# Performance work log

Hardware: AMD Instinct MI355X
Metric: run time of the kernel (lower is better)

The kernel has to match this reference:

```python
import jax, jax.numpy as jnp
import numpy as np

N = 100000      # nodes
E_RAND = 1500000
IN_DIM = 128
OUT_DIM = 128
H = 8
D = OUT_DIM // H  # 16 per-head dim
EPS = 1e-5


def _bn(x, gamma, beta):
    # BatchNorm1d, training mode: biased batch statistics over the node dim
    mu = jnp.mean(x, axis=0)
    var = jnp.mean((x - mu) ** 2, axis=0)
    return (x - mu) * jax.lax.rsqrt(var + EPS) * gamma + beta


def setup_inputs() -> dict:
    key = jax.random.key(0)
    ks = jax.random.split(key, 12)
    h = jax.random.normal(ks[0], (N, IN_DIM), dtype=jnp.float32)
    # edge list: random edges + self-loops so every dst has in-degree >= 1
    src_r = jax.random.randint(ks[1], (E_RAND,), 0, N, dtype=jnp.int32)
    dst_r = jax.random.randint(ks[2], (E_RAND,), 0, N, dtype=jnp.int32)
    loops = jnp.arange(N, dtype=jnp.int32)
    src = jnp.concatenate([loops, src_r])
    dst = jnp.concatenate([loops, dst_r])
    s = 1.0 / np.sqrt(IN_DIM)
    Wq = jax.random.normal(ks[3], (IN_DIM, OUT_DIM), dtype=jnp.float32) * s
    Wk = jax.random.normal(ks[4], (IN_DIM, OUT_DIM), dtype=jnp.float32) * s
    Wv = jax.random.normal(ks[5], (IN_DIM, OUT_DIM), dtype=jnp.float32) * s
    Wo = jax.random.normal(ks[6], (OUT_DIM, OUT_DIM), dtype=jnp.float32) * s
    bo = jnp.zeros((OUT_DIM,), dtype=jnp.float32)
    gamma1 = jnp.ones((OUT_DIM,), dtype=jnp.float32)
    beta1 = jnp.zeros((OUT_DIM,), dtype=jnp.float32)
    Wf1 = jax.random.normal(ks[7], (OUT_DIM, 2 * OUT_DIM), dtype=jnp.float32) * s
    bf1 = jnp.zeros((2 * OUT_DIM,), dtype=jnp.float32)
    Wf2 = jax.random.normal(ks[8], (2 * OUT_DIM, OUT_DIM), dtype=jnp.float32) * (1.0 / np.sqrt(2 * OUT_DIM))
    bf2 = jnp.zeros((OUT_DIM,), dtype=jnp.float32)
    gamma2 = jnp.ones((OUT_DIM,), dtype=jnp.float32)
    beta2 = jnp.zeros((OUT_DIM,), dtype=jnp.float32)
    return {"h": h, "Wq": Wq, "Wk": Wk, "Wv": Wv, "Wo": Wo, "bo": bo,
            "gamma1": gamma1, "beta1": beta1, "Wf1": Wf1, "bf1": bf1,
            "Wf2": Wf2, "bf2": bf2, "gamma2": gamma2, "beta2": beta2,
            "src": src, "dst": dst}


def reference(h, Wq, Wk, Wv, Wo, bo, gamma1, beta1, Wf1, bf1, Wf2, bf2,
              gamma2, beta2, src, dst):
    n = h.shape[0]
    Q = (h @ Wq).reshape(n, H, D)
    K = (h @ Wk).reshape(n, H, D)
    V = (h @ Wv).reshape(n, H, D)
    # per-edge score: (K[src] * Q[dst]).sum(-1), scaled exp with clamp
    score = jnp.sum(K[src] * Q[dst], axis=-1) / np.sqrt(D)   # [E, H]
    score = jnp.exp(jnp.clip(score, -5.0, 5.0))
    # weighted aggregation to dst nodes
    wV = jax.ops.segment_sum(V[src] * score[:, :, None], dst, num_segments=n)  # [N,H,D]
    z = jax.ops.segment_sum(score, dst, num_segments=n)                         # [N,H]
    attn = (wV / z[:, :, None]).reshape(n, OUT_DIM)
    # output projection + residual + batchnorm
    x = h + (attn @ Wo + bo)
    x = _bn(x, gamma1, beta1)
    # FFN + residual + batchnorm
    y = jax.nn.relu(x @ Wf1 + bf1) @ Wf2 + bf2
    x = _bn(x + y, gamma2, beta2)
    return x
```

## Files before the change

kernel.cpp:

```cpp
#include <hip/hip_runtime.h>

#define EPS 1e-5f
#define VSCALE 20.0f

typedef __attribute__((ext_vector_type(8))) short sh8;
typedef __attribute__((ext_vector_type(4))) float f4;
typedef __attribute__((ext_vector_type(2))) _Float16 h2f;

static __device__ __forceinline__ unsigned short f2b(float f) {
    union { float f; unsigned u; } v; v.f = f;
    unsigned r = v.u + 0x7FFF + ((v.u >> 16) & 1);
    return (unsigned short)(r >> 16);
}
static __device__ __forceinline__ float b2f(unsigned short b) {
    union { unsigned u; float f; } v; v.u = ((unsigned)b) << 16; return v.f;
}
static __device__ __forceinline__ unsigned pk2(float a, float b) {
    return (unsigned)f2b(a) | ((unsigned)f2b(b) << 16);
}
static __device__ __forceinline__ h2f u2h(unsigned u) {
    union { unsigned u; h2f h; } c; c.u = u; return c.h;
}
static __device__ __forceinline__ float dot2h(h2f a, h2f b, float c) {
#if __has_builtin(__builtin_amdgcn_fdot2)
    return __builtin_amdgcn_fdot2(a, b, c, false);
#else
    return (float)a.x * (float)b.x + (float)a.y * (float)b.y + c;
#endif
}
#if __has_builtin(__builtin_amdgcn_cvt_f32_ubyte0)
#define UB0(x) __builtin_amdgcn_cvt_f32_ubyte0(x)
#define UB1(x) __builtin_amdgcn_cvt_f32_ubyte1(x)
#define UB2(x) __builtin_amdgcn_cvt_f32_ubyte2(x)
#define UB3(x) __builtin_amdgcn_cvt_f32_ubyte3(x)
#else
#define UB0(x) ((float)((x) & 0xffu))
#define UB1(x) ((float)(((x) >> 8) & 0xffu))
#define UB2(x) ((float)(((x) >> 16) & 0xffu))
#define UB3(x) ((float)((x) >> 24))
#endif

static __device__ __forceinline__ void barrier_raw() {
    __builtin_amdgcn_sched_barrier(0);
    asm volatile("s_waitcnt lgkmcnt(0)" ::: "memory");
    __builtin_amdgcn_s_barrier();
    __builtin_amdgcn_sched_barrier(0);
}

__global__ __launch_bounds__(256) void prep_all_k(
    const float* __restrict__ Wq, const float* __restrict__ Wk,
    const float* __restrict__ Wv, const float* __restrict__ Wo,
    const float* __restrict__ Wf1, const float* __restrict__ Wf2,
    unsigned short* __restrict__ Wt)
{
    int i = blockIdx.x * 256 + threadIdx.x;
    if (i < 65536) {
        int s = i >> 14;
        const float* W = (s == 0) ? Wq : (s == 1) ? Wk : (s == 2) ? Wv : Wo;
        int l = i & 16383, k = l >> 7, n = l & 127;
        Wt[(i & ~16383) + n * 128 + k] = f2b(W[l]);
    } else if (i < 98304) {
        int l = i - 65536, k = l >> 8, n = l & 255;
        Wt[65536 + n * 128 + k] = f2b(Wf1[l]);
    } else {
        int l = i - 98304, k = l >> 7, n = l & 127;
        Wt[98304 + n * 256 + k] = f2b(Wf2[l]);
    }
}

__global__ __launch_bounds__(512, 4) void qkv3_k(
    const float* __restrict__ h, const unsigned short* __restrict__ Wt,
    _Float16* __restrict__ Qh, unsigned char* __restrict__ KV,
    int M, int tiles)
{
    constexpr int KD = 128, CPR = 16, PER = 2;
    __shared__ __align__(16) unsigned short Ws[128 * KD];
    __shared__ __align__(16) unsigned short As[2][64 * KD];
    const int tid = threadIdx.x;
    const int wave = tid >> 6, lane = tid & 63;
    const int q = lane >> 4, lm = lane & 15;
    const int wr = wave >> 2, wc = wave & 3;
    const int wv = blockIdx.y;
    const unsigned short* Wblk = Wt + (size_t)wv * 16384;

    float4 rAf[PER][2];
    {
        const int rowT = blockIdx.x * 64;
#pragma unroll
        for (int i = 0; i < PER; ++i) {
            int g = tid + i * 512;
            int row = g >> 4, ch = g & 15;
            int grow = rowT + row; if (grow >= M) grow = M - 1;
            const float* p = &h[(size_t)grow * 128 + ch * 8];
            rAf[i][0] = *(const float4*)p;
            rAf[i][1] = *(const float4*)(p + 4);
        }
    }

#pragma unroll
    for (int i = 0; i < 4; ++i) {
        int g = tid + i * 512;
        int col = g >> 4, ch = g & 15;
        uint4 v = *(const uint4*)&Wblk[(size_t)col * KD + ch * 8];
        *(uint4*)&Ws[col * KD + ((ch ^ (col & 7)) * 8)] = v;
    }

    int cur = 0;
    for (int t = blockIdx.x; t < tiles; t += gridDim.x) {
        const int rowT = t * 64;
        barrier_raw();
        unsigned short* Asc = As[cur];
#pragma unroll
        for (int i = 0; i < PER; ++i) {
            int g = tid + i * 512;
            int row = g >> 4, ch = g & 15;
            uint4 v;
            v.x = pk2(rAf[i][0].x, rAf[i][0].y);
            v.y = pk2(rAf[i][0].z, rAf[i][0].w);
            v.z = pk2(rAf[i][1].x, rAf[i][1].y);
            v.w = pk2(rAf[i][1].z, rAf[i][1].w);
            *(uint4*)&Asc[row * KD + ((ch ^ (row & 7)) * 8)] = v;
        }
        const int tn = t + (int)gridDim.x;
        if (tn < tiles) {
            const int rowTn = tn * 64;
#pragma unroll
            for (int i = 0; i < PER; ++i) {
                int g = tid + i * 512;
                int row = g >> 4, ch = g & 15;
                int grow = rowTn + row; if (grow >= M) grow = M - 1;
                const float* p = &h[(size_t)grow * 128 + ch * 8];
                rAf[i][0] = *(const float4*)p;
                rAf[i][1] = *(const float4*)(p + 4);
            }
        }
        barrier_raw();

        f4 acc[2][2];
#pragma unroll
        for (int mi = 0; mi < 2; ++mi)
#pragma unroll
            for (int ni = 0; ni < 2; ++ni) {
                f4 z = {0.f, 0.f, 0.f, 0.f};
                acc[mi][ni] = z;
            }
#pragma unroll
        for (int kc = 0; kc < 4; ++kc) {
            sh8 af[2], bfr[2];
#pragma unroll
            for (int mi = 0; mi < 2; ++mi) {
                const int row = wr * 32 + mi * 16 + lm;
                af[mi] = *(const sh8*)&Asc[row * KD + (((kc * 4 + q) ^ (row & 7)) * 8)];
            }
#pragma unroll
            for (int ni = 0; ni < 2; ++ni) {
                const int col = wc * 32 + ni * 16 + lm;
                bfr[ni] = *(const sh8*)&Ws[col * KD + (((kc * 4 + q) ^ (col & 7)) * 8)];
            }
#pragma unroll
            for (int mi = 0; mi < 2; ++mi)
#pragma unroll
                for (int ni = 0; ni < 2; ++ni)
                    acc[mi][ni] = __builtin_amdgcn_mfma_f32_16x16x32_bf16(
                        af[mi], bfr[ni], acc[mi][ni], 0, 0, 0);
        }

#pragma unroll
        for (int ni = 0; ni < 2; ++ni) {
            const int col = wc * 32 + ni * 16 + lm;
#pragma unroll
            for (int mi = 0; mi < 2; ++mi) {
#pragma unroll
                for (int r = 0; r < 4; ++r) {
                    const int row = rowT + wr * 32 + mi * 16 + q * 4 + r;
                    if (row >= M) continue;
                    const float v = acc[mi][ni][r];
                    if (wv == 0) Qh[(size_t)row * 128 + col] = (_Float16)v;
                    else if (wv == 1)
                        *(_Float16*)(KV + (size_t)row * 384 + col * 2) = (_Float16)v;
                    else {
                        float tt = rintf(v * VSCALE);
                        tt = fminf(fmaxf(tt, -127.f), 127.f);
                        KV[(size_t)row * 384 + 256 + col] = (unsigned char)(int)(tt + 128.f);
                    }
                }
            }
        }
        cur ^= 1;
    }
}

template<int KD, int RES, int STATS, int RELU>
__global__ __launch_bounds__(512) void gemm2_k(
    const unsigned short* __restrict__ A, const unsigned short* __restrict__ Wt,
    const float* __restrict__ bias, const void* __restrict__ resid,
    unsigned short* __restrict__ C, int M, int ldc, int tiles,
    const float* __restrict__ aff1, float* __restrict__ ostats)
{
    constexpr int CPR = KD / 8;
    constexpr int PER = 64 * CPR / 512;
    __shared__ __align__(16) unsigned short Ws[128 * KD];
    __shared__ __align__(16) unsigned short As[2][64 * KD];
    __shared__ float sacc[256];
    const int tid = threadIdx.x;
    const int wave = tid >> 6, lane = tid & 63;
    const int q = lane >> 4, lm = lane & 15;
    const int wr = wave >> 2, wc = wave & 3;
    const int colBase = blockIdx.y * 128;
    const unsigned short* Wblk = Wt + (size_t)colBase * KD;

    uint4 rA[PER];
    {
        const int rowT = blockIdx.x * 64;
#pragma unroll
        for (int i = 0; i < PER; ++i) {
            int g = tid + i * 512;
            int row = g / CPR, ch = g % CPR;
            int grow = rowT + row; if (grow >= M) grow = M - 1;
            rA[i] = *(const uint4*)&A[(size_t)grow * KD + ch * 8];
        }
    }

#pragma unroll
    for (int i = 0; i < 128 * CPR / 512; ++i) {
        int g = tid + i * 512;
        int col = g / CPR, ch = g % CPR;
        uint4 v = *(const uint4*)&Wblk[(size_t)col * KD + ch * 8];
        *(uint4*)&Ws[col * KD + ((ch ^ (col & 7)) * 8)] = v;
    }
    if (STATS && tid < 256) sacc[tid] = 0.f;

    float bv[2], rsc[2], rsh[2];
#pragma unroll
    for (int ni = 0; ni < 2; ++ni) {
        const int col = colBase + wc * 32 + ni * 16 + lm;
        bv[ni] = bias[col];
        if (RES == 3) { rsc[ni] = aff1[col]; rsh[ni] = aff1[128 + col]; }
        else { rsc[ni] = 0.f; rsh[ni] = 0.f; }
    }
    float st_s[2] = {0.f, 0.f}, st_ss[2] = {0.f, 0.f};

    int cur = 0;
    for (int t = blockIdx.x; t < tiles; t += gridDim.x) {
        const int rowT = t * 64;
        barrier_raw();
        unsigned short* Asc = As[cur];
#pragma unroll
        for (int i = 0; i < PER; ++i) {
            int g = tid + i * 512;
            int row = g / CPR, ch = g % CPR;
            *(uint4*)&Asc[row * KD + ((ch ^ (row & 7)) * 8)] = rA[i];
        }
        const int tn = t + (int)gridDim.x;
        if (tn < tiles) {
            const int rowTn = tn * 64;
#pragma unroll
            for (int i = 0; i < PER; ++i) {
                int g = tid + i * 512;
                int row = g / CPR, ch = g % CPR;
                int grow = rowTn + row; if (grow >= M) grow = M - 1;
                rA[i] = *(const uint4*)&A[(size_t)grow * KD + ch * 8];
            }
        }
        barrier_raw();

        f4 acc[2][2];
#pragma unroll
        for (int mi = 0; mi < 2; ++mi)
#pragma unroll
            for (int ni = 0; ni < 2; ++ni) {
                f4 z = {0.f, 0.f, 0.f, 0.f};
                acc[mi][ni] = z;
            }
#pragma unroll
        for (int kc = 0; kc < KD / 32; ++kc) {
            sh8 af[2], bfr[2];
#pragma unroll
            for (int mi = 0; mi < 2; ++mi) {
                const int row = wr * 32 + mi * 16 + lm;
                af[mi] = *(const sh8*)&Asc[row * KD + (((kc * 4 + q) ^ (row & 7)) * 8)];
            }
#pragma unroll
            for (int ni = 0; ni < 2; ++ni) {
                const int col = wc * 32 + ni * 16 + lm;
                bfr[ni] = *(const sh8*)&Ws[col * KD + (((kc * 4 + q) ^ (col & 7)) * 8)];
            }
#pragma unroll
            for (int mi = 0; mi < 2; ++mi)
#pragma unroll
                for (int ni = 0; ni < 2; ++ni)
                    acc[mi][ni] = __builtin_amdgcn_mfma_f32_16x16x32_bf16(
                        af[mi], bfr[ni], acc[mi][ni], 0, 0, 0);
        }

#pragma unroll
        for (int ni = 0; ni < 2; ++ni) {
            const int col = colBase + wc * 32 + ni * 16 + lm;
#pragma unroll
            for (int mi = 0; mi < 2; ++mi) {
#pragma unroll
                for (int r = 0; r < 4; ++r) {
                    const int row = rowT + wr * 32 + mi * 16 + q * 4 + r;
                    if (row >= M) continue;
                    float val = acc[mi][ni][r] + bv[ni];
                    if (RES == 1)
                        val += ((const float*)resid)[(size_t)row * ldc + col];
                    if (RES == 3)
                        val += b2f(((const unsigned short*)resid)[(size_t)row * ldc + col])
                               * rsc[ni] + rsh[ni];
                    if (RELU) val = fmaxf(val, 0.f);
                    if (STATS) { st_s[ni] += val; st_ss[ni] += val * val; }
                    C[(size_t)row * ldc + col] = f2b(val);
                }
            }
        }
        cur ^= 1;
    }

    if (STATS) {
        barrier_raw();
#pragma unroll
        for (int ni = 0; ni < 2; ++ni) {
            st_s[ni]  += __shfl_xor(st_s[ni], 16);  st_s[ni]  += __shfl_xor(st_s[ni], 32);
            st_ss[ni] += __shfl_xor(st_ss[ni], 16); st_ss[ni] += __shfl_xor(st_ss[ni], 32);
            if (q == 0) {
                const int c = wc * 32 + ni * 16 + lm;
                atomicAdd(&sacc[c], st_s[ni]);
                atomicAdd(&sacc[128 + c], st_ss[ni]);
            }
        }
        barrier_raw();
        if (tid < 128) {
            atomicAdd(&ostats[tid], sacc[tid]);
            atomicAdd(&ostats[128 + tid], sacc[128 + tid]);
        }
    }
}

__global__ __launch_bounds__(256) void fold_bn1_k(
    const unsigned short* __restrict__ W1t, const float* __restrict__ rstats,
    const float* __restrict__ g1, const float* __restrict__ b1,
    const float* __restrict__ bf1, float invN,
    unsigned short* __restrict__ W1f, float* __restrict__ b1f,
    float* __restrict__ aff1)
{
    __shared__ float sc[128], sh[128];
    const int t = threadIdx.x;
    if (t < 128) {
        const float mu = rstats[t] * invN;
        const float var = rstats[128 + t] * invN - mu * mu;
        const float isg = rsqrtf(var + EPS) * g1[t];
        const float shf = b1[t] - mu * isg;
        sc[t] = isg; sh[t] = shf;
        aff1[t] = isg; aff1[128 + t] = shf;
    }
    __syncthreads();
    float acc = bf1[t];
#pragma unroll
    for (int c = 0; c < 128; c += 8) {
        const uint4 v = *(const uint4*)&W1t[t * 128 + c];
        const float w0 = b2f((unsigned short)(v.x & 0xffff));
        const float w1 = b2f((unsigned short)(v.x >> 16));
        const float w2 = b2f((unsigned short)(v.y & 0xffff));
        const float w3 = b2f((unsigned short)(v.y >> 16));
        const float w4 = b2f((unsigned short)(v.z & 0xffff));
        const float w5 = b2f((unsigned short)(v.z >> 16));
        const float w6 = b2f((unsigned short)(v.w & 0xffff));
        const float w7 = b2f((unsigned short)(v.w >> 16));
        acc += sh[c] * w0 + sh[c + 1] * w1 + sh[c + 2] * w2 + sh[c + 3] * w3
             + sh[c + 4] * w4 + sh[c + 5] * w5 + sh[c + 6] * w6 + sh[c + 7] * w7;
        uint4 o;
        o.x = pk2(w0 * sc[c],     w1 * sc[c + 1]);
        o.y = pk2(w2 * sc[c + 2], w3 * sc[c + 3]);
        o.z = pk2(w4 * sc[c + 4], w5 * sc[c + 5]);
        o.w = pk2(w6 * sc[c + 6], w7 * sc[c + 7]);
        *(uint4*)&W1f[t * 128 + c] = o;
    }
    b1f[t] = acc;
}

__global__ __launch_bounds__(256) void bucket_cnt_k(const int* __restrict__ dst,
                                                    int E, int* __restrict__ bCnt)
{
    __shared__ int c[512];
    const int t = threadIdx.x;
    c[t] = 0; c[t + 256] = 0;
    __syncthreads();
    for (int i = blockIdx.x * 256 + t; i < E; i += gridDim.x * 256)
        atomicAdd(&c[dst[i] >> 8], 1);
    __syncthreads();
    if (c[t]) atomicAdd(&bCnt[t], c[t]);
    if (c[t + 256]) atomicAdd(&bCnt[t + 256], c[t + 256]);
}

__global__ __launch_bounds__(512) void bucket_scan_k(const int* __restrict__ bCnt,
                                                     int B, int* __restrict__ bOff,
                                                     int* __restrict__ bCur)
{
    __shared__ int ts[512];
    const int t = threadIdx.x;
    const int v = (t < B) ? bCnt[t] : 0;
    ts[t] = v;
    __syncthreads();
    for (int o = 1; o < 512; o <<= 1) {
        int u = (t >= o) ? ts[t - o] : 0;
        __syncthreads();
        ts[t] += u;
        __syncthreads();
    }
    const int ex = ts[t] - v;
    if (t < B) { bOff[t] = ex; bCur[t] = ex; }
    if (t == B - 1) bOff[B] = ex + v;
}

#define CCH 8192
__global__ __launch_bounds__(512) void coarse_k(const int* __restrict__ src,
                                                const int* __restrict__ dst, int E,
                                                int* __restrict__ bCur,
                                                unsigned* __restrict__ coarse)
{
    __shared__ int cnt[512], off[512], gbase[512], rc[512];
    __shared__ unsigned pk[CCH];
    __shared__ int ga[CCH];
    const int t = threadIdx.x;
    const int e0 = blockIdx.x * CCH;
    const int n = min(CCH, E - e0);
    cnt[t] = 0;
    __syncthreads();
    for (int i = t; i < n; i += 512) atomicAdd(&cnt[dst[e0 + i] >> 8], 1);
    __syncthreads();
    const int v = cnt[t];
    off[t] = v;
    __syncthreads();
    for (int o = 1; o < 512; o <<= 1) {
        int u = (t >= o) ? off[t - o] : 0;
        __syncthreads();
        off[t] += u;
        __syncthreads();
    }
    const int ex = off[t] - v;
    off[t] = ex;
    if (v > 0) gbase[t] = atomicAdd(&bCur[t], v);
    rc[t] = 0;
    __syncthreads();
    for (int i = t; i < n; i += 512) {
        const int d = dst[e0 + i], s = src[e0 + i];
        const int b = d >> 8;
        const int j = atomicAdd(&rc[b], 1);
        const int slot = off[b] + j;
        pk[slot] = ((unsigned)(d & 255) << 17) | (unsigned)s;
        ga[slot] = gbase[b] + j;
    }
    __syncthreads();
    for (int i = t; i < n; i += 512) coarse[ga[i]] = pk[i];
}

__global__ __launch_bounds__(256) void fine_k(const unsigned* __restrict__ coarse,
                                              const int* __restrict__ bOff, int B,
                                              int Nn, int* __restrict__ row_ptr,
                                              int* __restrict__ esrc)
{
    __shared__ int cnt[256], off[256], rc[256];
    const int t = threadIdx.x;
    const int b = blockIdx.x;
    const int base = b << 8;
    const int e0 = bOff[b], e1 = bOff[b + 1];
    cnt[t] = 0;
    __syncthreads();
    for (int i = e0 + t; i < e1; i += 256)
        atomicAdd(&cnt[(coarse[i] >> 17) & 255], 1);
    __syncthreads();
    const int v = cnt[t];
    off[t] = v;
    __syncthreads();
    for (int o = 1; o < 256; o <<= 1) {
        int u = (t >= o) ? off[t - o] : 0;
        __syncthreads();
        off[t] += u;
        __syncthreads();
    }
    const int ex = off[t] - v;
    off[t] = ex;
    rc[t] = 0;
    if (base + t < Nn) row_ptr[base + t] = e0 + ex;
    if (b == B - 1 && t == 0) row_ptr[Nn] = e1;
    __syncthreads();
    for (int i = e0 + t; i < e1; i += 256) {
        const unsigned p = coarse[i];
        const int l = (p >> 17) & 255;
        const int j = atomicAdd(&rc[l], 1);
        esrc[e0 + off[l] + j] = (int)(p & 0x1FFFFu);
    }
}

#define EA_ACC(kc, vc, EI) do {                                              \
    float sp = dot2h(u2h((kc).w), q3, dot2h(u2h((kc).z), q2,                 \
               dot2h(u2h((kc).y), q1, dot2h(u2h((kc).x), q0, 0.f))));        \
    sp += __shfl_xor(sp, 1);                                                 \
    float sc = __expf(fminf(fmaxf(sp * 0.25f, -5.f), 5.f));                  \
    sc = ((EI) < nb) ? sc : 0.f;                                             \
    a0 += sc * UB0((vc).x);                                                  \
    a1 += sc * UB1((vc).x);                                                  \
    a2 += sc * UB2((vc).x);                                                  \
    a3 += sc * UB3((vc).x);                                                  \
    a4 += sc * UB0((vc).y);                                                  \
    a5 += sc * UB1((vc).y);                                                  \
    a6 += sc * UB2((vc).y);                                                  \
    a7 += sc * UB3((vc).y);                                                  \
    z += sc;                                                                 \
} while (0)

__global__ __launch_bounds__(256) void edge_attn_k(
    const _Float16* __restrict__ Qh, const unsigned char* __restrict__ KV,
    const int* __restrict__ row_ptr, const int* __restrict__ esrc,
    unsigned short* __restrict__ attnb, int nodeOff, int nodeEnd)
{
    const int wave = threadIdx.x >> 6, lane = threadIdx.x & 63;
    const int node = nodeOff + blockIdx.x * 4 + wave;
    if (node >= nodeEnd) return;
    const int g = lane & 15, p = lane >> 4;
    const uint4 qv = *(const uint4*)&Qh[(size_t)node * 128 + g * 8];
    const h2f q0 = u2h(qv.x), q1 = u2h(qv.y), q2 = u2h(qv.z), q3 = u2h(qv.w);
    const int e0 = row_ptr[node], e1 = row_ptr[node + 1];
    const int cnt = e1 - e0;
    const int e1m1 = e1 - 1;
    float a0 = 0.f, a1 = 0.f, a2 = 0.f, a3 = 0.f;
    float a4 = 0.f, a5 = 0.f, a6 = 0.f, a7 = 0.f, z = 0.f;
    for (int base = 0; base < cnt; base += 64) {
        const int nb = min(cnt - base, 64);
        const int eb = e0 + base + p;
        {
            const int s0 = esrc[min(eb, e1m1)];
            const unsigned char* r = KV + (size_t)((unsigned)s0 * 384u);
            const int s1 = esrc[min(eb + 4, e1m1)];
            const unsigned char* rB = KV + (size_t)((unsigned)s1 * 384u);
            uint4 kvA = *(const uint4*)(r + g * 16);
            uint2 vvA = *(const uint2*)(r + 256 + g * 8);
            uint4 kvB = *(const uint4*)(rB + g * 16);
            uint2 vvB = *(const uint2*)(rB + 256 + g * 8);
            for (int j = 0; j < nb; j += 8) {
                {
                    const uint4 kc = kvA; const uint2 vc = vvA;
                    if (j + 8 < nb) {
                        const int sn = esrc[min(eb + j + 8, e1m1)];
                        const unsigned char* rn = KV + (size_t)((unsigned)sn * 384u);
                        kvA = *(const uint4*)(rn + g * 16);
                        vvA = *(const uint2*)(rn + 256 + g * 8);
                    }
                    EA_ACC(kc, vc, j + p);
                }
                {
                    const uint4 kc = kvB; const uint2 vc = vvB;
                    if (j + 12 < nb) {
                        const int sn = esrc[min(eb + j + 12, e1m1)];
                        const unsigned char* rn = KV + (size_t)((unsigned)sn * 384u);
                        kvB = *(const uint4*)(rn + g * 16);
                        vvB = *(const uint2*)(rn + 256 + g * 8);
                    }
                    EA_ACC(kc, vc, j + 4 + p);
                }
            }
        }
    }
    a0 += __shfl_xor(a0, 16); a0 += __shfl_xor(a0, 32);
    a1 += __shfl_xor(a1, 16); a1 += __shfl_xor(a1, 32);
    a2 += __shfl_xor(a2, 16); a2 += __shfl_xor(a2, 32);
    a3 += __shfl_xor(a3, 16); a3 += __shfl_xor(a3, 32);
    a4 += __shfl_xor(a4, 16); a4 += __shfl_xor(a4, 32);
    a5 += __shfl_xor(a5, 16); a5 += __shfl_xor(a5, 32);
    a6 += __shfl_xor(a6, 16); a6 += __shfl_xor(a6, 32);
    a7 += __shfl_xor(a7, 16); a7 += __shfl_xor(a7, 32);
    z  += __shfl_xor(z, 16);  z  += __shfl_xor(z, 32);
    const float inv = 1.f / (z * VSCALE);
    const float c = 128.f * z;
    if (p == 0) {
        uint4 o;
        o.x = pk2((a0 - c) * inv, (a1 - c) * inv);
        o.y = pk2((a2 - c) * inv, (a3 - c) * inv);
        o.z = pk2((a4 - c) * inv, (a5 - c) * inv);
        o.w = pk2((a6 - c) * inv, (a7 - c) * inv);
        *(uint4*)&attnb[(size_t)node * 128 + g * 8] = o;
    }
}

__global__ __launch_bounds__(256) void bn_apply_b_k(const unsigned short* __restrict__ X,
                                                    const float* __restrict__ rstats,
                                                    const float* __restrict__ gma,
                                                    const float* __restrict__ bta,
                                                    float invN, int total8,
                                                    float* __restrict__ out)
{
    __shared__ float aff[256];
    if (threadIdx.x < 128) {
        const int c = threadIdx.x;
        const float mu = rstats[c] * invN;
        const float var = rstats[128 + c] * invN - mu * mu;
        const float isg = rsqrtf(var + EPS) * gma[c];
        aff[c] = isg;
        aff[128 + c] = bta[c] - mu * isg;
    }
    __syncthreads();
    for (int i = blockIdx.x * blockDim.x + threadIdx.x; i < total8;
         i += gridDim.x * blockDim.x) {
        const int c8 = (i & 15) * 8;
        const float4 sc0 = *(const float4*)&aff[c8];
        const float4 sc1 = *(const float4*)&aff[c8 + 4];
        const float4 sh0 = *(const float4*)&aff[128 + c8];
        const float4 sh1 = *(const float4*)&aff[128 + c8 + 4];
        const uint4 v = ((const uint4*)X)[i];
        float4 o0, o1;
        o0.x = b2f((unsigned short)(v.x & 0xffff)) * sc0.x + sh0.x;
        o0.y = b2f((unsigned short)(v.x >> 16))    * sc0.y + sh0.y;
        o0.z = b2f((unsigned short)(v.y & 0xffff)) * sc0.z + sh0.z;
        o0.w = b2f((unsigned short)(v.y >> 16))    * sc0.w + sh0.w;
        o1.x = b2f((unsigned short)(v.z & 0xffff)) * sc1.x + sh1.x;
        o1.y = b2f((unsigned short)(v.z >> 16))    * sc1.y + sh1.y;
        o1.z = b2f((unsigned short)(v.w & 0xffff)) * sc1.z + sh1.z;
        o1.w = b2f((unsigned short)(v.w >> 16))    * sc1.w + sh1.w;
        ((float4*)out)[i * 2]     = o0;
        ((float4*)out)[i * 2 + 1] = o1;
    }
}

extern "C" void kernel_launch(void* const* d_in, const int* in_sizes, int n_in,
                              void* d_out, int out_size, void* d_ws, size_t ws_size,
                              hipStream_t stream)
{
    const float* h   = (const float*)d_in[0];
    const float* Wq  = (const float*)d_in[1];
    const float* Wk  = (const float*)d_in[2];
    const float* Wv  = (const float*)d_in[3];
    const float* Wo  = (const float*)d_in[4];
    const float* bo  = (const float*)d_in[5];
    const float* g1  = (const float*)d_in[6];
    const float* b1  = (const float*)d_in[7];
    const float* Wf1 = (const float*)d_in[8];
    const float* bf1 = (const float*)d_in[9];
    const float* Wf2 = (const float*)d_in[10];
    const float* bf2 = (const float*)d_in[11];
    const float* g2  = (const float*)d_in[12];
    const float* b2  = (const float*)d_in[13];
    const int*   src = (const int*)d_in[14];
    const int*   dstv= (const int*)d_in[15];
    const int N = in_sizes[0] / 128;
    const int E = in_sizes[14];
    const int B = (N + 255) >> 8;
    const float invN = 1.f / (float)N;

    unsigned short* Wt = (unsigned short*)d_ws;
    float* stats1 = (float*)((char*)d_ws + 262144);
    float* stats2 = stats1 + 256;
    int* bCnt = (int*)(stats2 + 256);
    int* bOff = bCnt + 512;
    int* bCur = bOff + 513;
    uintptr_t big = ((uintptr_t)(bCur + 512) + 255) & ~(uintptr_t)255;
    _Float16* Qh = (_Float16*)big;
    unsigned char* KV = (unsigned char*)(Qh + (size_t)N * 128);
    uintptr_t a2 = ((uintptr_t)(KV + (size_t)N * 384) + 255) & ~(uintptr_t)255;
    unsigned short* attnb = (unsigned short*)a2;
    unsigned short* xb = attnb + (size_t)N * 128;
    int* row_ptr = (int*)(xb + (size_t)N * 128);
    unsigned* coarse = (unsigned*)attnb;
    int* esrc = (int*)xb;
    unsigned short* hidden = (unsigned short*)Qh;
    unsigned short* yb = attnb;
    uintptr_t fb = (big + (size_t)N * 512 + 255) & ~(uintptr_t)255;
    float* aff1 = (float*)fb;
    float* b1f  = aff1 + 256;
    unsigned short* W1f = (unsigned short*)(b1f + 256);

    unsigned short* Wf1T = Wt + 65536;
    unsigned short* Wf2T = Wt + 98304;

    float* out = (float*)d_out;
    const dim3 b256(256);
    const dim3 b512(512);
    const int tiles64 = (N + 63) / 64;

    hipMemsetAsync(stats1, 0, 4096, stream);

    prep_all_k<<<dim3(512), b256, 0, stream>>>(Wq, Wk, Wv, Wo, Wf1, Wf2, Wt);

    bucket_cnt_k<<<dim3(256), b256, 0, stream>>>(dstv, E, bCnt);
    bucket_scan_k<<<dim3(1), dim3(512), 0, stream>>>(bCnt, B, bOff, bCur);
    coarse_k<<<dim3((E + CCH - 1) / CCH), dim3(512), 0, stream>>>(src, dstv, E, bCur, coarse);
    fine_k<<<dim3(B), b256, 0, stream>>>(coarse, bOff, B, N, row_ptr, esrc);

    qkv3_k<<<dim3(171, 3), b512, 0, stream>>>(h, Wt, Qh, KV, N, tiles64);

    {
        const int c1 = ((N / 3) + 3) & ~3;
        const int c2 = ((2 * N / 3) + 3) & ~3;
        edge_attn_k<<<dim3((c1 + 3) / 4), b256, 0, stream>>>(
            Qh, KV, row_ptr, esrc, attnb, 0, c1);
        edge_attn_k<<<dim3((c2 - c1 + 3) / 4), b256, 0, stream>>>(
            Qh, KV, row_ptr, esrc, attnb, c1, c2);
        edge_attn_k<<<dim3((N - c2 + 3) / 4), b256, 0, stream>>>(
            Qh, KV, row_ptr, esrc, attnb, c2, N);
    }

    gemm2_k<128, 1, 1, 0><<<dim3(512, 1), b512, 0, stream>>>(
        attnb, Wt + 49152, bo, h, xb, N, 128, tiles64, nullptr, stats1);

    fold_bn1_k<<<dim3(1), b256, 0, stream>>>(Wf1T, stats1, g1, b1, bf1, invN,
                                             W1f, b1f, aff1);

    gemm2_k<128, 0, 0, 1><<<dim3(512, 2), b512, 0, stream>>>(
        xb, W1f, b1f, nullptr, hidden, N, 256, tiles64, nullptr, nullptr);

    gemm2_k<256, 3, 1, 0><<<dim3(256, 1), b512, 0, stream>>>(
        hidden, Wf2T, bf2, xb, yb, N, 128, tiles64, aff1, stats2);

    bn_apply_b_k<<<dim3(1024), b256, 0, stream>>>(yb, stats2, g2, b2, invN, N * 16, out);
}
```

Baseline: 485.5 us.

## Hold weight MFMA fragments in registers instead of LDS in GEMM kernels

The QKV and dense GEMM kernels now load each wave's weight B-fragments straight from global memory into registers once, and drop the 32-64 KB weight tile in shared memory. This removes the per-k-step LDS reads of weights and frees shared memory, so launch bounds are raised to 8 blocks per CU and grids are enlarged to use the extra occupancy. The cost is more VGPRs per thread (up to 16 sh8 fragments for KD=256), which may spill or cap occupancy below the requested level, and weight loads from global memory are no longer coalesced through a swizzled layout.

```diff
diff --git a/kernel.cpp b/kernel.cpp
--- a/kernel.cpp
+++ b/kernel.cpp
@@ -68,13 +68,12 @@
     }
 }
 
-__global__ __launch_bounds__(512, 4) void qkv3_k(
+__global__ __launch_bounds__(512, 8) void qkv3_k(
     const float* __restrict__ h, const unsigned short* __restrict__ Wt,
     _Float16* __restrict__ Qh, unsigned char* __restrict__ KV,
     int M, int tiles)
 {
-    constexpr int KD = 128, CPR = 16, PER = 2;
-    __shared__ __align__(16) unsigned short Ws[128 * KD];
+    constexpr int KD = 128, PER = 2;
     __shared__ __align__(16) unsigned short As[2][64 * KD];
     const int tid = threadIdx.x;
     const int wave = tid >> 6, lane = tid & 63;
@@ -97,13 +96,13 @@
         }
     }
 
-#pragma unroll
-    for (int i = 0; i < 4; ++i) {
-        int g = tid + i * 512;
-        int col = g >> 4, ch = g & 15;
-        uint4 v = *(const uint4*)&Wblk[(size_t)col * KD + ch * 8];
-        *(uint4*)&Ws[col * KD + ((ch ^ (col & 7)) * 8)] = v;
-    }
+    sh8 wfr[2][4];
+#pragma unroll
+    for (int ni = 0; ni < 2; ++ni)
+#pragma unroll
+        for (int kc = 0; kc < 4; ++kc)
+            wfr[ni][kc] = *(const sh8*)&Wblk[(size_t)(wc * 32 + ni * 16 + lm) * KD
+                                             + (kc * 4 + q) * 8];
 
     int cur = 0;
     for (int t = blockIdx.x; t < tiles; t += gridDim.x) {
@@ -146,23 +145,18 @@
             }
 #pragma unroll
         for (int kc = 0; kc < 4; ++kc) {
-            sh8 af[2], bfr[2];
+            sh8 af[2];
 #pragma unroll
             for (int mi = 0; mi < 2; ++mi) {
                 const int row = wr * 32 + mi * 16 + lm;
                 af[mi] = *(const sh8*)&Asc[row * KD + (((kc * 4 + q) ^ (row & 7)) * 8)];
             }
 #pragma unroll
-            for (int ni = 0; ni < 2; ++ni) {
-                const int col = wc * 32 + ni * 16 + lm;
-                bfr[ni] = *(const sh8*)&Ws[col * KD + (((kc * 4 + q) ^ (col & 7)) * 8)];
-            }
-#pragma unroll
             for (int mi = 0; mi < 2; ++mi)
 #pragma unroll
                 for (int ni = 0; ni < 2; ++ni)
                     acc[mi][ni] = __builtin_amdgcn_mfma_f32_16x16x32_bf16(
-                        af[mi], bfr[ni], acc[mi][ni], 0, 0, 0);
+                        af[mi], wfr[ni][kc], acc[mi][ni], 0, 0, 0);
         }
 
 #pragma unroll
@@ -191,7 +185,7 @@
 }
 
 template<int KD, int RES, int STATS, int RELU>
-__global__ __launch_bounds__(512) void gemm2_k(
+__global__ __launch_bounds__(512, 8) void gemm3_k(
     const unsigned short* __restrict__ A, const unsigned short* __restrict__ Wt,
     const float* __restrict__ bias, const void* __restrict__ resid,
     unsigned short* __restrict__ C, int M, int ldc, int tiles,
@@ -199,7 +193,7 @@
 {
     constexpr int CPR = KD / 8;
     constexpr int PER = 64 * CPR / 512;
-    __shared__ __align__(16) unsigned short Ws[128 * KD];
+    constexpr int KC = KD / 32;
     __shared__ __align__(16) unsigned short As[2][64 * KD];
     __shared__ float sacc[256];
     const int tid = threadIdx.x;
@@ -221,13 +215,13 @@
         }
     }
 
-#pragma unroll
-    for (int i = 0; i < 128 * CPR / 512; ++i) {
-        int g = tid + i * 512;
-        int col = g / CPR, ch = g % CPR;
-        uint4 v = *(const uint4*)&Wblk[(size_t)col * KD + ch * 8];
-        *(uint4*)&Ws[col * KD + ((ch ^ (col & 7)) * 8)] = v;
-    }
+    sh8 wfr[2][KC];
+#pragma unroll
+    for (int ni = 0; ni < 2; ++ni)
+#pragma unroll
+        for (int kc = 0; kc < KC; ++kc)
+            wfr[ni][kc] = *(const sh8*)&Wblk[(size_t)(wc * 32 + ni * 16 + lm) * KD
+                                             + (kc * 4 + q) * 8];
     if (STATS && tid < 256) sacc[tid] = 0.f;
 
     float bv[2], rsc[2], rsh[2];
@@ -273,24 +267,19 @@
                 acc[mi][ni] = z;
             }
 #pragma unroll
-        for (int kc = 0; kc < KD / 32; ++kc) {
-            sh8 af[2], bfr[2];
+        for (int kc = 0; kc < KC; ++kc) {
+            sh8 af[2];
 #pragma unroll
             for (int mi = 0; mi < 2; ++mi) {
                 const int row = wr * 32 + mi * 16 + lm;
                 af[mi] = *(const sh8*)&Asc[row * KD + (((kc * 4 + q) ^ (row & 7)) * 8)];
             }
 #pragma unroll
-            for (int ni = 0; ni < 2; ++ni) {
-                const int col = wc * 32 + ni * 16 + lm;
-                bfr[ni] = *(const sh8*)&Ws[col * KD + (((kc * 4 + q) ^ (col & 7)) * 8)];
-            }
-#pragma unroll
             for (int mi = 0; mi < 2; ++mi)
 #pragma unroll
                 for (int ni = 0; ni < 2; ++ni)
                     acc[mi][ni] = __builtin_amdgcn_mfma_f32_16x16x32_bf16(
-                        af[mi], bfr[ni], acc[mi][ni], 0, 0, 0);
+                        af[mi], wfr[ni][kc], acc[mi][ni], 0, 0, 0);
         }
 
 #pragma unroll
@@ -686,7 +675,7 @@
     coarse_k<<<dim3((E + CCH - 1) / CCH), dim3(512), 0, stream>>>(src, dstv, E, bCur, coarse);
     fine_k<<<dim3(B), b256, 0, stream>>>(coarse, bOff, B, N, row_ptr, esrc);
 
-    qkv3_k<<<dim3(171, 3), b512, 0, stream>>>(h, Wt, Qh, KV, N, tiles64);
+    qkv3_k<<<dim3(341, 3), b512, 0, stream>>>(h, Wt, Qh, KV, N, tiles64);
 
     {
         const int c1 = ((N / 3) + 3) & ~3;
@@ -699,16 +688,16 @@
             Qh, KV, row_ptr, esrc, attnb, c2, N);
     }
 
-    gemm2_k<128, 1, 1, 0><<<dim3(512, 1), b512, 0, stream>>>(
+    gemm3_k<128, 1, 1, 0><<<dim3(512, 1), b512, 0, stream>>>(
         attnb, Wt + 49152, bo, h, xb, N, 128, tiles64, nullptr, stats1);
 
     fold_bn1_k<<<dim3(1), b256, 0, stream>>>(Wf1T, stats1, g1, b1, bf1, invN,
                                              W1f, b1f, aff1);
 
-    gemm2_k<128, 0, 0, 1><<<dim3(512, 2), b512, 0, stream>>>(
+    gemm3_k<128, 0, 0, 1><<<dim3(512, 2), b512, 0, stream>>>(
         xb, W1f, b1f, nullptr, hidden, N, 256, tiles64, nullptr, nullptr);
 
-    gemm2_k<256, 3, 1, 0><<<dim3(256, 1), b512, 0, stream>>>(
+    gemm3_k<256, 3, 1, 0><<<dim3(512, 1), b512, 0, stream>>>(
         hidden, Wf2T, bf2, xb, yb, N, 128, tiles64, aff1, stats2);
 
     bn_apply_b_k<<<dim3(1024), b256, 0, stream>>>(yb, stats2, g2, b2, invN, N * 16, out);
```

New measurement: 561.3 us. 1.16x slower.
